# Performance work log

Hardware: AMD Instinct MI355X
Metric: run time of the kernel (lower is better)

Reference implementation:

```python
import jax, jax.numpy as jnp
import numpy as np

B, S, DIM = 2, 2048, 2048
H, QLR, KVLR = 16, 1536, 512
D_NOPE, D_ROPE, D_QK, D_V = 128, 64, 192, 128
EPS = 1e-6


def rms_norm(x, w, eps=EPS):
    return x * jax.lax.rsqrt(jnp.mean(jnp.square(x), axis=-1, keepdims=True) + eps) * w


def rope(x, theta):
    # x: [b, s, n, d], theta: [s, d//2] rotation angles
    xr = x.reshape(*x.shape[:-1], -1, 2)
    x0, x1 = xr[..., 0], xr[..., 1]
    cos = jnp.cos(theta)[None, :, None, :]
    sin = jnp.sin(theta)[None, :, None, :]
    out = jnp.stack([x0 * cos - x1 * sin, x0 * sin + x1 * cos], axis=-1)
    return out.reshape(x.shape).astype(x.dtype)


def setup_inputs() -> dict:
    key = jax.random.key(0)
    ks = jax.random.split(key, 6)
    x = jax.random.normal(ks[0], (B, S, DIM), jnp.float32)
    # standard RoPE angles theta[s, i] = s / 10000^(2i/d_rope)
    pos = jnp.arange(S, dtype=jnp.float32)
    inv = 1.0 / (10000.0 ** (jnp.arange(0, D_ROPE, 2, dtype=jnp.float32) / D_ROPE))
    freqs = pos[:, None] * inv[None, :]  # [S, D_ROPE//2]
    sc = lambda k, shp: jax.random.normal(k, shp, jnp.float32) * (1.0 / np.sqrt(shp[0]))
    return {
        'x': x,
        'freqs': freqs,
        'start_pos': 0,
        'wq_a': sc(ks[1], (DIM, QLR)),
        'q_norm_w': jnp.ones((QLR,), jnp.float32),
        'wq_b': sc(ks[2], (QLR, H * D_QK)),
        'wkv_a': sc(ks[3], (DIM, KVLR + D_ROPE)),
        'kv_norm_w': jnp.ones((KVLR,), jnp.float32),
        'wkv_b': sc(ks[4], (KVLR, H * (D_NOPE + D_V))),
        'wo': sc(ks[5], (H * D_V, DIM)),
    }


def reference(x, freqs, start_pos, wq_a, q_norm_w, wq_b, wkv_a, kv_norm_w, wkv_b, wo):
    bsz, seqlen, _ = x.shape
    scale = D_QK ** -0.5
    # low-rank Q: down-proj -> RMSNorm -> up-proj
    q = rms_norm(x @ wq_a, q_norm_w) @ wq_b
    q = q.reshape(bsz, seqlen, H, D_QK)
    q_nope, q_pe = q[..., :D_NOPE], q[..., D_NOPE:]
    q_pe = rope(q_pe, freqs)
    # low-rank KV: joint down-proj, split latent / rope part
    kv = x @ wkv_a
    c_kv, k_pe = kv[..., :KVLR], kv[..., KVLR:]
    k_pe = rope(k_pe[:, :, None, :], freqs)[:, :, 0, :]  # [b, t, r]
    # weight absorption: fold wkv_b's k_nope block into q
    wkv_b_mat = wkv_b.T.reshape(H, D_NOPE + D_V, KVLR)  # [h, d_nope+d_v, c]
    q_abs = jnp.einsum('bshd,hdc->bshc', q_nope, wkv_b_mat[:, :D_NOPE])
    kv_cache = rms_norm(c_kv, kv_norm_w)  # [b, t, c] compressed KV cache
    scores = (jnp.einsum('bshc,btc->bsht', q_abs, kv_cache)
              + jnp.einsum('bshr,btr->bsht', q_pe, k_pe)) * scale
    causal = jnp.tril(jnp.ones((seqlen, seqlen), bool))  # prefill, start_pos=0
    scores = jnp.where(causal[None, :, None, :], scores, -1e9)
    attn = jax.nn.softmax(scores.astype(jnp.float32), axis=-1).astype(x.dtype)
    # attend in latent space, then up-project with the v block of wkv_b
    o = jnp.einsum('bsht,btc->bshc', attn, kv_cache)
    o = jnp.einsum('bshc,hdc->bshd', o, wkv_b_mat[:, D_NOPE:])
    return o.reshape(bsz, seqlen, H * D_V) @ wo
```

## Files before the change

### kernel.cpp

```cpp
#include <hip/hip_runtime.h>

typedef __bf16 bf16x8 __attribute__((ext_vector_type(8)));
typedef float floatx4 __attribute__((ext_vector_type(4)));

#define MFMA(a, b, c) __builtin_amdgcn_mfma_f32_16x16x32_bf16((a), (b), (c), 0, 0, 0)

__device__ __forceinline__ float bf2f(ushort u) {
    union { unsigned int i; float f; } v; v.i = ((unsigned int)u) << 16; return v.f;
}
__device__ __forceinline__ ushort f2bf(float f) {
    union { float f; unsigned int i; } v; v.f = f;
    unsigned int r = v.i + 0x7fffu + ((v.i >> 16) & 1u);
    return (ushort)(r >> 16);
}
__device__ __forceinline__ bf16x8 ldb8(const ushort* p) { return *(const bf16x8*)p; }

__global__ __launch_bounds__(256) void transpose_f32_bf16(
    const float* __restrict__ in, ushort* __restrict__ out, int R, int C) {
    __shared__ ushort tile[32][33];
    const int c0 = blockIdx.x * 32, r0 = blockIdx.y * 32;
    const int tx = threadIdx.x, ty = threadIdx.y;
    #pragma unroll
    for (int i = 0; i < 32; i += 8) {
        int r = r0 + ty + i, c = c0 + tx;
        if (r < R && c < C) tile[ty + i][tx] = f2bf(in[(long)r * C + c]);
    }
    __syncthreads();
    #pragma unroll
    for (int i = 0; i < 32; i += 8) {
        int r = c0 + ty + i, c = r0 + tx;
        if (r < C && c < R) out[(long)r * R + c] = tile[tx][ty + i];
    }
}

__global__ __launch_bounds__(256) void cvt_f32_bf16(
    const float* __restrict__ in, ushort* __restrict__ out, long n) {
    const long i = ((long)blockIdx.x * 256 + threadIdx.x) * 4;
    if (i >= n) return;
    float4 v = *(const float4*)(in + i);
    ushort4 o;
    o.x = f2bf(v.x); o.y = f2bf(v.y); o.z = f2bf(v.z); o.w = f2bf(v.w);
    *(ushort4*)(out + i) = o;
}

__global__ __launch_bounds__(256) void trigtab(
    const float* __restrict__ freqs, float2* __restrict__ trig) {
    const int idx = blockIdx.x * 256 + threadIdx.x;
    float th = freqs[idx];
    trig[idx] = make_float2(cosf(th), sinf(th));
}

__global__ __launch_bounds__(256, 2) void gemm_bt128(
    const ushort* __restrict__ A, const ushort* __restrict__ Bt,
    void* __restrict__ C, int K, int lda, int ldb, int ldc,
    long aZ, long bZ, long cZ, int c_f32) {
    __shared__ __align__(16) ushort As[128 * 64];
    __shared__ __align__(16) ushort Bs[128 * 64];
    const int z = blockIdx.z;
    const ushort* Ab = A + (long)z * aZ;
    const ushort* Bb = Bt + (long)z * bZ;
    const long m0 = (long)blockIdx.y * 128;
    const long n0 = (long)blockIdx.x * 128;
    const int tid = threadIdx.x;
    const int lane = tid & 63, w = tid >> 6;
    const int wm = (w >> 1) * 64, wn = (w & 1) * 64;
    const int lrow = lane & 15, quad = lane >> 4;

    floatx4 acc[4][4] = {};

    for (int k0 = 0; k0 < K; k0 += 64) {
        __syncthreads();
        #pragma unroll
        for (int t = 0; t < 4; ++t) {
            const int c = t * 256 + tid;
            const int r = c >> 3, kc = (c & 7) * 8;
            __builtin_amdgcn_global_load_lds(
                (const __attribute__((address_space(1))) unsigned int*)(Ab + (m0 + r) * lda + k0 + kc),
                (__attribute__((address_space(3))) unsigned int*)(As + (long)c * 8), 16, 0, 0);
            __builtin_amdgcn_global_load_lds(
                (const __attribute__((address_space(1))) unsigned int*)(Bb + (n0 + r) * ldb + k0 + kc),
                (__attribute__((address_space(3))) unsigned int*)(Bs + (long)c * 8), 16, 0, 0);
        }
        __syncthreads();
        #pragma unroll
        for (int kk = 0; kk < 64; kk += 32) {
            bf16x8 af[4], bv[4];
            #pragma unroll
            for (int i = 0; i < 4; ++i) {
                af[i] = ldb8(&As[(wm + i * 16 + lrow) * 64 + kk + quad * 8]);
                bv[i] = ldb8(&Bs[(wn + i * 16 + lrow) * 64 + kk + quad * 8]);
            }
            #pragma unroll
            for (int i = 0; i < 4; ++i)
                #pragma unroll
                for (int j = 0; j < 4; ++j)
                    acc[i][j] = MFMA(af[i], bv[j], acc[i][j]);
        }
    }
    if (c_f32) {
        float* Cb = (float*)C + (long)z * cZ;
        #pragma unroll
        for (int mt = 0; mt < 4; ++mt)
            #pragma unroll
            for (int nt = 0; nt < 4; ++nt)
                #pragma unroll
                for (int r = 0; r < 4; ++r)
                    Cb[(m0 + wm + mt * 16 + quad * 4 + r) * ldc + n0 + wn + nt * 16 + lrow] = acc[mt][nt][r];
    } else {
        ushort* Cb = (ushort*)C + (long)z * cZ;
        #pragma unroll
        for (int mt = 0; mt < 4; ++mt)
            #pragma unroll
            for (int nt = 0; nt < 4; ++nt)
                #pragma unroll
                for (int r = 0; r < 4; ++r)
                    Cb[(m0 + wm + mt * 16 + quad * 4 + r) * ldc + n0 + wn + nt * 16 + lrow] = f2bf(acc[mt][nt][r]);
    }
}

__global__ __launch_bounds__(256) void rms1536(
    ushort* qk, const float* __restrict__ w) {
    const int row = blockIdx.x, t = threadIdx.x;
    const int lane = t & 63, wv = t >> 6;
    ushort* ip = qk + (long)row * 2176;
    float v[6]; float ss = 0.f;
    #pragma unroll
    for (int i = 0; i < 6; ++i) { v[i] = bf2f(ip[i * 256 + t]); ss += v[i] * v[i]; }
    #pragma unroll
    for (int off = 32; off > 0; off >>= 1) ss += __shfl_xor(ss, off);
    __shared__ float red[4];
    if (lane == 0) red[wv] = ss;
    __syncthreads();
    const float tot = red[0] + red[1] + red[2] + red[3];
    const float sc = rsqrtf(tot * (1.f / 1536.f) + 1e-6f);
    #pragma unroll
    for (int i = 0; i < 6; ++i) ip[i * 256 + t] = f2bf(v[i] * sc * w[i * 256 + t]);
}

__global__ __launch_bounds__(256) void qrope(
    const ushort* __restrict__ q, const float2* __restrict__ trig,
    ushort* __restrict__ qpe) {
    const int tok = blockIdx.x;
    const int s = tok & 2047;
    const int t = threadIdx.x;
    #pragma unroll
    for (int p = 0; p < 2; ++p) {
        const int idx = p * 256 + t;
        const int h = idx >> 5, i = idx & 31;
        const long base = (long)tok * 3072 + h * 192 + 128 + 2 * i;
        float x0 = bf2f(q[base]), x1 = bf2f(q[base + 1]);
        float2 cs = trig[s * 32 + i];
        const long ob = (long)tok * 1024 + h * 64 + 2 * i;
        qpe[ob]     = f2bf(x0 * cs.x - x1 * cs.y);
        qpe[ob + 1] = f2bf(x0 * cs.y + x1 * cs.x);
    }
}

__global__ __launch_bounds__(256) void kvprep(
    const ushort* __restrict__ qk, const float* __restrict__ w,
    const float2* __restrict__ trig, ushort* __restrict__ kvc,
    ushort* __restrict__ kpe) {
    const int tok = blockIdx.x;
    const int s = tok & 2047;
    const int t = threadIdx.x;
    const int lane = t & 63, wv = t >> 6;
    const ushort* in2 = qk + (long)tok * 2176 + 1536;
    const float v0 = bf2f(in2[t]);
    const float v1 = bf2f(in2[256 + t]);
    float ss = v0 * v0 + v1 * v1;
    #pragma unroll
    for (int off = 32; off > 0; off >>= 1) ss += __shfl_xor(ss, off);
    __shared__ float red[4];
    if (lane == 0) red[wv] = ss;
    __syncthreads();
    const float tot = red[0] + red[1] + red[2] + red[3];
    const float sc = rsqrtf(tot * (1.f / 512.f) + 1e-6f);
    kvc[(long)tok * 512 + t] = f2bf(v0 * sc * w[t]);
    kvc[(long)tok * 512 + 256 + t] = f2bf(v1 * sc * w[256 + t]);
    if (t < 32) {
        float x0 = bf2f(in2[512 + 2 * t]);
        float x1 = bf2f(in2[512 + 2 * t + 1]);
        float2 cs = trig[s * 32 + t];
        kpe[(long)tok * 64 + 2 * t]     = f2bf(x0 * cs.x - x1 * cs.y);
        kpe[(long)tok * 64 + 2 * t + 1] = f2bf(x0 * cs.y + x1 * cs.x);
    }
}

__global__ __launch_bounds__(256, 2) void mha_attn(
    const ushort* __restrict__ q,
    const ushort* __restrict__ qpe,
    const ushort* __restrict__ kn,
    const ushort* __restrict__ kpe,
    const ushort* __restrict__ vT,
    ushort* __restrict__ o2) {
    __shared__ __align__(16) ushort Ks[128][200];
    __shared__ __align__(16) ushort P[64][136];
    const int fid = blockIdx.x + (blockIdx.y << 4) + (blockIdx.z << 8);
    const int xcd = fid & 7, j = fid >> 3;
    const int g = xcd * 4 + (j >> 4);
    const int qx = j & 15, h = g & 15, b = g >> 4;
    const int tid = threadIdx.x, lane = tid & 63, w = tid >> 6;
    const int lrow = lane & 15, quad = lane >> 4;
    const long bb = (long)b * 2048;
    const float scale = 0.07216878364870323f * 1.4426950408889634f;
    const int rn = tid >> 4, cn = (tid & 15) * 8;
    const int rr = tid >> 3, cr = (tid & 7) * 8;

    for (int half = 0; half < 2; ++half) {
        const int qt = half ? (31 - qx) : qx;
        const int qrow = qt * 64;
        const long tokb = bb + qrow;

        bf16x8 qa[6];
        {
            const ushort* qp_ = q + (tokb + w * 16 + lrow) * 3072 + h * 192 + quad * 8;
            #pragma unroll
            for (int ks = 0; ks < 4; ++ks) qa[ks] = ldb8(qp_ + ks * 32);
            const ushort* qq = qpe + (tokb + w * 16 + lrow) * 1024 + h * 64 + quad * 8;
            qa[4] = ldb8(qq); qa[5] = ldb8(qq + 32);
        }

        floatx4 oacc[4][2] = {};
        float m_i[4], l_i[4];
        #pragma unroll
        for (int r = 0; r < 4; ++r) { m_i[r] = -1e30f; l_i[r] = 0.f; }

        const int niter = qt / 2 + 1;
        for (int t = 0; t < niter; ++t) {
            const int kv0 = t * 128;
            {
                const ushort* src = kn + (bb + kv0 + rn) * 2048 + h * 128 + cn;
                #pragma unroll
                for (int j2 = 0; j2 < 8; ++j2) {
                    uint4 v = *(const uint4*)(src + (long)j2 * 16 * 2048);
                    *(uint4*)&Ks[j2 * 16 + rn][cn] = v;
                }
                const ushort* srp = kpe + (bb + kv0 + rr) * 64 + cr;
                #pragma unroll
                for (int j2 = 0; j2 < 4; ++j2) {
                    uint4 v = *(const uint4*)(srp + (long)j2 * 32 * 64);
                    *(uint4*)&Ks[j2 * 32 + rr][128 + cr] = v;
                }
            }
            __syncthreads();

            floatx4 sacc[8] = {};
            __builtin_amdgcn_s_setprio(1);
            #pragma unroll
            for (int f = 0; f < 8; ++f)
                #pragma unroll
                for (int ks = 0; ks < 6; ++ks)
                    sacc[f] = MFMA(qa[ks], ldb8(&Ks[f * 16 + lrow][ks * 32 + quad * 8]), sacc[f]);
            __builtin_amdgcn_s_setprio(0);

            bf16x8 vf[2][4];
            {
                const ushort* vb = vT + ((long)(b * 16 + h)) * 262144 + (long)(w * 32 + lrow) * 2048 + kv0 + quad * 8;
                #pragma unroll
                for (int nf = 0; nf < 2; ++nf)
                    #pragma unroll
                    for (int kk = 0; kk < 4; ++kk)
                        vf[nf][kk] = ldb8(vb + (long)nf * 16 * 2048 + kk * 32);
            }

            #pragma unroll
            for (int r = 0; r < 4; ++r) {
                const int rloc = w * 16 + quad * 4 + r;
                const int row_s = qrow + rloc;
                float pv[8];
                float smax = -1e30f;
                #pragma unroll
                for (int f = 0; f < 8; ++f) {
                    pv[f] = sacc[f][r] * scale;
                    if (kv0 + f * 16 + lrow > row_s) pv[f] = -1e30f;
                    smax = fmaxf(smax, pv[f]);
                }
                #pragma unroll
                for (int off = 1; off < 16; off <<= 1)
                    smax = fmaxf(smax, __shfl_xor(smax, off));
                const float mnew = fmaxf(m_i[r], smax);
                const float alpha = __builtin_amdgcn_exp2f(m_i[r] - mnew);
                float ps = 0.f;
                #pragma unroll
                for (int f = 0; f < 8; ++f) {
                    float p = __builtin_amdgcn_exp2f(pv[f] - mnew);
                    P[rloc][f * 16 + lrow] = f2bf(p);
                    ps += p;
                }
                #pragma unroll
                for (int off = 1; off < 16; off <<= 1)
                    ps += __shfl_xor(ps, off);
                l_i[r] = l_i[r] * alpha + ps;
                m_i[r] = mnew;
                if (lrow == 0) *(float*)&P[rloc][128] = alpha;
            }
            __syncthreads();

            __builtin_amdgcn_s_setprio(1);
            #pragma unroll
            for (int mf = 0; mf < 4; ++mf) {
                float al[4];
                #pragma unroll
                for (int r = 0; r < 4; ++r) al[r] = *(const float*)&P[mf * 16 + quad * 4 + r][128];
                const int need = (al[0] != 1.f) | (al[1] != 1.f) | (al[2] != 1.f) | (al[3] != 1.f);
                if (__any(need)) {
                    #pragma unroll
                    for (int nf = 0; nf < 2; ++nf)
                        #pragma unroll
                        for (int r = 0; r < 4; ++r) oacc[mf][nf][r] *= al[r];
                }
                #pragma unroll
                for (int kk = 0; kk < 4; ++kk) {
                    bf16x8 pf = ldb8(&P[mf * 16 + lrow][kk * 32 + quad * 8]);
                    oacc[mf][0] = MFMA(pf, vf[0][kk], oacc[mf][0]);
                    oacc[mf][1] = MFMA(pf, vf[1][kk], oacc[mf][1]);
                }
            }
            __builtin_amdgcn_s_setprio(0);
        }

        #pragma unroll
        for (int r = 0; r < 4; ++r)
            if (lrow == 0) *(float*)&P[w * 16 + quad * 4 + r][132] = l_i[r];
        __syncthreads();
        #pragma unroll
        for (int mf = 0; mf < 4; ++mf) {
            float li[4];
            #pragma unroll
            for (int r = 0; r < 4; ++r) li[r] = *(const float*)&P[mf * 16 + quad * 4 + r][132];
            #pragma unroll
            for (int nf = 0; nf < 2; ++nf)
                #pragma unroll
                for (int r = 0; r < 4; ++r) {
                    long tok = tokb + mf * 16 + quad * 4 + r;
                    o2[tok * 2048 + h * 128 + w * 32 + nf * 16 + lrow] = f2bf(oacc[mf][nf][r] / li[r]);
                }
        }
        __syncthreads();
    }
}

extern "C" void kernel_launch(void* const* d_in, const int* in_sizes, int n_in,
                              void* d_out, int out_size, void* d_ws, size_t ws_size,
                              hipStream_t stream) {
    const float* x      = (const float*)d_in[0];
    const float* freqs  = (const float*)d_in[1];
    const float* wq_a   = (const float*)d_in[3];
    const float* qnw    = (const float*)d_in[4];
    const float* wq_b   = (const float*)d_in[5];
    const float* wkv_a  = (const float*)d_in[6];
    const float* kvnw   = (const float*)d_in[7];
    const float* wkv_b  = (const float*)d_in[8];
    const float* wo     = (const float*)d_in[9];
    float* out = (float*)d_out;
    (void)ws_size; (void)in_sizes; (void)n_in; (void)out_size;

    char* ws = (char*)d_ws;
    ushort* qk_comb = (ushort*)(ws + 0);
    ushort* o2      = (ushort*)(ws + 0);
    ushort* xb      = (ushort*)(ws + 17825792);
    ushort* knope   = (ushort*)(ws + 17825792);
    ushort* q       = (ushort*)(ws + 34603008);
    ushort* qpe     = (ushort*)(ws + 59768832);
    ushort* kvc     = (ushort*)(ws + 68157440);
    ushort* kpe     = (ushort*)(ws + 72351744);
    ushort* vT      = (ushort*)(ws + 72876032);
    ushort* wcombT  = (ushort*)(ws + 89653248);
    ushort* wq_bT   = (ushort*)(ws + 98566144);
    ushort* wkv_bT  = (ushort*)(ws + 108003328);
    ushort* woT     = (ushort*)(ws + 112197632);
    float2* trig    = (float2*)(ws + 120586240);

    dim3 tb(32, 8);
    trigtab<<<256, 256, 0, stream>>>(freqs, trig);
    transpose_f32_bf16<<<dim3(48, 64), tb, 0, stream>>>(wq_a, wcombT, 2048, 1536);
    transpose_f32_bf16<<<dim3(18, 64), tb, 0, stream>>>(wkv_a, wcombT + 1536L * 2048, 2048, 576);
    transpose_f32_bf16<<<dim3(96, 48), tb, 0, stream>>>(wq_b, wq_bT, 1536, 3072);
    transpose_f32_bf16<<<dim3(128, 16), tb, 0, stream>>>(wkv_b, wkv_bT, 512, 4096);
    transpose_f32_bf16<<<dim3(64, 64), tb, 0, stream>>>(wo, woT, 2048, 2048);
    cvt_f32_bf16<<<8192, 256, 0, stream>>>(x, xb, 8388608L);

    gemm_bt128<<<dim3(17, 32, 1), 256, 0, stream>>>(xb, wcombT, qk_comb, 2048, 2048, 2048, 2176, 0, 0, 0, 0);
    rms1536<<<4096, 256, 0, stream>>>(qk_comb, qnw);
    gemm_bt128<<<dim3(24, 32, 1), 256, 0, stream>>>(qk_comb, wq_bT, q, 1536, 2176, 1536, 3072, 0, 0, 0, 0);
    qrope<<<4096, 256, 0, stream>>>(q, trig, qpe);
    kvprep<<<4096, 256, 0, stream>>>(qk_comb, kvnw, trig, kvc, kpe);

    gemm_bt128<<<dim3(1, 16, 16), 256, 0, stream>>>(kvc, wkv_bT, knope,
        512, 512, 512, 2048, 0, 131072, 128, 0);
    gemm_bt128<<<dim3(1, 16, 16), 256, 0, stream>>>(kvc + 1048576, wkv_bT, knope + 4194304,
        512, 512, 512, 2048, 0, 131072, 128, 0);
    gemm_bt128<<<dim3(16, 1, 16), 256, 0, stream>>>(wkv_bT + 65536, kvc, vT,
        512, 512, 512, 2048, 131072, 0, 262144, 0);
    gemm_bt128<<<dim3(16, 1, 16), 256, 0, stream>>>(wkv_bT + 65536, kvc + 1048576, vT + 4194304,
        512, 512, 512, 2048, 131072, 0, 262144, 0);

    mha_attn<<<dim3(16, 16, 2), 256, 0, stream>>>(q, qpe, knope, kpe, vT, o2);

    gemm_bt128<<<dim3(16, 32, 1), 256, 0, stream>>>(o2, woT, out, 2048, 2048, 2048, 2048, 0, 0, 0, 1);
}
```

Before: 488.1 us.

## Prefetch K tiles into registers, skip mask off-diagonal, merge knope GEMM launches

The attention kernel now issues global loads for the next K tile into registers before the QK MFMAs and writes them to shared memory after the softmax barrier. This overlaps load latency with compute. The causal mask is now applied only on the diagonal tile, the GEMM launch bound is raised to request 3 blocks per SIMD, and the two per-batch knope GEMMs are merged into one launch covering both batches. Holding the prefetched K tile raises register pressure, and the occupancy hint may force spills in the GEMM.

```diff
diff --git a/kernel.cpp b/kernel.cpp
--- a/kernel.cpp
+++ b/kernel.cpp
@@ -50,7 +50,7 @@
     trig[idx] = make_float2(cosf(th), sinf(th));
 }
 
-__global__ __launch_bounds__(256, 2) void gemm_bt128(
+__global__ __launch_bounds__(256, 3) void gemm_bt128(
     const ushort* __restrict__ A, const ushort* __restrict__ Bt,
     void* __restrict__ C, int K, int lda, int ldb, int ldc,
     long aZ, long bZ, long cZ, int c_f32) {
@@ -226,32 +226,33 @@
         for (int r = 0; r < 4; ++r) { m_i[r] = -1e30f; l_i[r] = 0.f; }
 
         const int niter = qt / 2 + 1;
+
+        {
+            const ushort* src = kn + (bb + rn) * 2048 + h * 128 + cn;
+            #pragma unroll
+            for (int j2 = 0; j2 < 8; ++j2)
+                *(uint4*)&Ks[j2 * 16 + rn][cn] = *(const uint4*)(src + (long)j2 * 16 * 2048);
+            const ushort* srp = kpe + (bb + rr) * 64 + cr;
+            #pragma unroll
+            for (int j2 = 0; j2 < 4; ++j2)
+                *(uint4*)&Ks[j2 * 32 + rr][128 + cr] = *(const uint4*)(srp + (long)j2 * 32 * 64);
+        }
+
         for (int t = 0; t < niter; ++t) {
             const int kv0 = t * 128;
-            {
-                const ushort* src = kn + (bb + kv0 + rn) * 2048 + h * 128 + cn;
-                #pragma unroll
-                for (int j2 = 0; j2 < 8; ++j2) {
-                    uint4 v = *(const uint4*)(src + (long)j2 * 16 * 2048);
-                    *(uint4*)&Ks[j2 * 16 + rn][cn] = v;
-                }
-                const ushort* srp = kpe + (bb + kv0 + rr) * 64 + cr;
-                #pragma unroll
-                for (int j2 = 0; j2 < 4; ++j2) {
-                    uint4 v = *(const uint4*)(srp + (long)j2 * 32 * 64);
-                    *(uint4*)&Ks[j2 * 32 + rr][128 + cr] = v;
-                }
-            }
             __syncthreads();
 
-            floatx4 sacc[8] = {};
-            __builtin_amdgcn_s_setprio(1);
-            #pragma unroll
-            for (int f = 0; f < 8; ++f)
-                #pragma unroll
-                for (int ks = 0; ks < 6; ++ks)
-                    sacc[f] = MFMA(qa[ks], ldb8(&Ks[f * 16 + lrow][ks * 32 + quad * 8]), sacc[f]);
-            __builtin_amdgcn_s_setprio(0);
+            uint4 knx[8], kpx[4];
+            const bool pf = (t + 1 < niter);
+            if (pf) {
+                const int kv1 = kv0 + 128;
+                const ushort* src = kn + (bb + kv1 + rn) * 2048 + h * 128 + cn;
+                #pragma unroll
+                for (int j2 = 0; j2 < 8; ++j2) knx[j2] = *(const uint4*)(src + (long)j2 * 16 * 2048);
+                const ushort* srp = kpe + (bb + kv1 + rr) * 64 + cr;
+                #pragma unroll
+                for (int j2 = 0; j2 < 4; ++j2) kpx[j2] = *(const uint4*)(srp + (long)j2 * 32 * 64);
+            }
 
             bf16x8 vf[2][4];
             {
@@ -263,6 +264,16 @@
                         vf[nf][kk] = ldb8(vb + (long)nf * 16 * 2048 + kk * 32);
             }
 
+            floatx4 sacc[8] = {};
+            __builtin_amdgcn_s_setprio(1);
+            #pragma unroll
+            for (int f = 0; f < 8; ++f)
+                #pragma unroll
+                for (int ks = 0; ks < 6; ++ks)
+                    sacc[f] = MFMA(qa[ks], ldb8(&Ks[f * 16 + lrow][ks * 32 + quad * 8]), sacc[f]);
+            __builtin_amdgcn_s_setprio(0);
+
+            const bool diag = (t == niter - 1);
             #pragma unroll
             for (int r = 0; r < 4; ++r) {
                 const int rloc = w * 16 + quad * 4 + r;
@@ -272,7 +283,7 @@
                 #pragma unroll
                 for (int f = 0; f < 8; ++f) {
                     pv[f] = sacc[f][r] * scale;
-                    if (kv0 + f * 16 + lrow > row_s) pv[f] = -1e30f;
+                    if (diag) { if (kv0 + f * 16 + lrow > row_s) pv[f] = -1e30f; }
                     smax = fmaxf(smax, pv[f]);
                 }
                 #pragma unroll
@@ -295,6 +306,13 @@
                 if (lrow == 0) *(float*)&P[rloc][128] = alpha;
             }
             __syncthreads();
+
+            if (pf) {
+                #pragma unroll
+                for (int j2 = 0; j2 < 8; ++j2) *(uint4*)&Ks[j2 * 16 + rn][cn] = knx[j2];
+                #pragma unroll
+                for (int j2 = 0; j2 < 4; ++j2) *(uint4*)&Ks[j2 * 32 + rr][128 + cr] = kpx[j2];
+            }
 
             __builtin_amdgcn_s_setprio(1);
             #pragma unroll
@@ -311,9 +329,9 @@
                 }
                 #pragma unroll
                 for (int kk = 0; kk < 4; ++kk) {
-                    bf16x8 pf = ldb8(&P[mf * 16 + lrow][kk * 32 + quad * 8]);
-                    oacc[mf][0] = MFMA(pf, vf[0][kk], oacc[mf][0]);
-                    oacc[mf][1] = MFMA(pf, vf[1][kk], oacc[mf][1]);
+                    bf16x8 pf2 = ldb8(&P[mf * 16 + lrow][kk * 32 + quad * 8]);
+                    oacc[mf][0] = MFMA(pf2, vf[0][kk], oacc[mf][0]);
+                    oacc[mf][1] = MFMA(pf2, vf[1][kk], oacc[mf][1]);
                 }
             }
             __builtin_amdgcn_s_setprio(0);
@@ -386,9 +404,7 @@
     qrope<<<4096, 256, 0, stream>>>(q, trig, qpe);
     kvprep<<<4096, 256, 0, stream>>>(qk_comb, kvnw, trig, kvc, kpe);
 
-    gemm_bt128<<<dim3(1, 16, 16), 256, 0, stream>>>(kvc, wkv_bT, knope,
-        512, 512, 512, 2048, 0, 131072, 128, 0);
-    gemm_bt128<<<dim3(1, 16, 16), 256, 0, stream>>>(kvc + 1048576, wkv_bT, knope + 4194304,
+    gemm_bt128<<<dim3(1, 32, 16), 256, 0, stream>>>(kvc, wkv_bT, knope,
         512, 512, 512, 2048, 0, 131072, 128, 0);
     gemm_bt128<<<dim3(16, 1, 16), 256, 0, stream>>>(wkv_bT + 65536, kvc, vT,
         512, 512, 512, 2048, 131072, 0, 262144, 0);
```

Measured after the change: 555.1 us. 13.7% more time.
